# Performance work log

Measured on AMD Instinct MI355X. Metric: run time of the kernel, lower is better.

Reference implementation:

```python
import jax, jax.numpy as jnp
import numpy as np

HEAD_SIZE = 128
B, L = 4, 4096

def setup_inputs() -> dict:
    key = jax.random.key(0)
    k1, k2, k3 = jax.random.split(key, 3)
    return {
        "key": jax.random.normal(k1, (B, L, HEAD_SIZE), dtype=jnp.float32),
        "query": jax.random.normal(k2, (B, L, HEAD_SIZE), dtype=jnp.float32),
        "value": jax.random.normal(k3, (B, L, HEAD_SIZE), dtype=jnp.float32),
    }

def reference(key, query, value):
    # attention scores: [B, L, L]
    scale = 1.0 / jnp.sqrt(jnp.asarray(HEAD_SIZE, dtype=query.dtype))
    att = jnp.einsum("bqd,bkd->bqk", query, key) * scale
    # causal mask (tril): positions k > q get -inf
    causal = jnp.tril(jnp.ones((att.shape[1], att.shape[2]), dtype=bool))
    att = jnp.where(causal[None, :, :], att, jnp.array(-jnp.inf, dtype=att.dtype))
    logits = jax.nn.softmax(att, axis=-1)
    # dropout omitted (eval mode / deterministic reference)
    out = jnp.einsum("bqk,bkd->bqd", logits, value)
    return out
```

## Files before the change

### kernel.cpp

```cpp
#include <hip/hip_runtime.h>

#define BB 4
#define LL 4096
#define DD 128

typedef __attribute__((ext_vector_type(8))) short short8;
typedef __attribute__((ext_vector_type(4))) float f32x4;

typedef __attribute__((address_space(1))) const unsigned int gas_u32;
typedef __attribute__((address_space(3))) unsigned int las_u32;

__device__ __forceinline__ void gload_lds16(const void* g, void* l) {
  __builtin_amdgcn_global_load_lds((gas_u32*)g, (las_u32*)l, 16, 0, 0);
}

__device__ __forceinline__ unsigned short f2bf(float x) {
  union { float f; unsigned int u; } c; c.f = x;
  unsigned int r = (c.u + 0x7FFFu + ((c.u >> 16) & 1u)) >> 16;
  return (unsigned short)r;
}
__device__ __forceinline__ float bf2f(unsigned short h) {
  union { unsigned int u; float f; } c; c.u = (unsigned int)h << 16;
  return c.f;
}

__host__ __device__ __forceinline__ int slotBase(int p) {
  int g2 = (p - 4) >> 2, w2 = (p - 4) & 3;
  return 2 * g2 * g2 + 6 * g2 + w2 * (g2 + 2);
}

__global__ __launch_bounds__(256) void prep(const float* __restrict__ K,
                                            const float* __restrict__ V,
                                            unsigned short* __restrict__ Kb,
                                            unsigned short* __restrict__ Vt) {
  __shared__ unsigned short tile[64 * 130];
  int b  = blockIdx.x >> 6;
  int kt = (blockIdx.x & 63) << 6;
  int t = threadIdx.x;
  {
    int key = t >> 2, part = t & 3;
    const float* src = K + ((size_t)b * LL + kt + key) * DD + part * 32;
    unsigned short* dst = Kb + ((size_t)b * LL + kt + key) * DD + part * 32;
#pragma unroll
    for (int j = 0; j < 4; ++j) {
      float4 x = *(const float4*)(src + j * 8);
      float4 y = *(const float4*)(src + j * 8 + 4);
      union { unsigned short h[8]; uint4 v; } o;
      o.h[0] = f2bf(x.x); o.h[1] = f2bf(x.y); o.h[2] = f2bf(x.z); o.h[3] = f2bf(x.w);
      o.h[4] = f2bf(y.x); o.h[5] = f2bf(y.y); o.h[6] = f2bf(y.z); o.h[7] = f2bf(y.w);
      *(uint4*)(dst + j * 8) = o.v;
    }
  }
  int keyi = t >> 5, dim = (t & 31) * 4;
#pragma unroll
  for (int j = 0; j < 8; ++j) {
    int key = keyi + j * 8;
    float4 x = *(const float4*)(V + ((size_t)b * LL + kt + key) * DD + dim);
    uint2 pk;
    pk.x = f2bf(x.x) | ((unsigned int)f2bf(x.y) << 16);
    pk.y = f2bf(x.z) | ((unsigned int)f2bf(x.w) << 16);
    *(uint2*)(tile + key * 130 + dim) = pk;
  }
  __syncthreads();
  int kg = (t & 7) * 8, d0 = t >> 3;
#pragma unroll
  for (int j = 0; j < 4; ++j) {
    int d = d0 + j * 32;
    union { unsigned short h[8]; uint4 v; } o;
#pragma unroll
    for (int i = 0; i < 8; ++i) o.h[i] = tile[(kg + i) * 130 + d];
    *(uint4*)(Vt + ((size_t)b * DD + d) * LL + kt + kg) = o.v;
  }
}

__global__ __launch_bounds__(256, 3) void attn_fwd(const float* __restrict__ Q,
                                                   const unsigned short* __restrict__ Kb,
                                                   const unsigned short* __restrict__ Vt,
                                                   float* __restrict__ Out,
                                                   unsigned short* __restrict__ partO,
                                                   float* __restrict__ stats,
                                                   int split) {
  __shared__ unsigned short Ks[64 * 128];
  __shared__ unsigned short Vs[128 * 64];
  __shared__ unsigned short Ps[4][32 * 72];

  int tid = threadIdx.x;
  int wave = tid >> 6;
  int lane = tid & 63;
  int l = lane & 15, gq = lane >> 4;
  int lx = l & 7;

  int rem = (int)blockIdx.x, p = 31, nch;
  while (true) {
    nch = split ? ((2 * p + 2 + 7) >> 3) : 1;
    int n = 4 * nch;
    if (rem < n) break;
    rem -= n; --p;
  }
  int b = rem / nch, c = rem % nch;
  int T = 2 * p + 2;
  int nIters = split ? min(8, T - c * 8) : T;
  int ktBase = c << 9;
  int q0w = (p << 7) + wave * 32;
  int wkend = q0w + 31;
  int slot = (split && nch > 1) ? (b * 140 + slotBase(p) + c) : 0;

  const float SC = 0.08838834764831845f * 1.4426950408889634f;
  short8 qf[2][4];
#pragma unroll
  for (int mt = 0; mt < 2; ++mt) {
    const float* qp = Q + ((size_t)b * LL + q0w + mt * 16 + l) * DD + gq * 8;
#pragma unroll
    for (int cc = 0; cc < 4; ++cc) {
      float4 x = *(const float4*)(qp + cc * 32);
      float4 y = *(const float4*)(qp + cc * 32 + 4);
      short8 f;
      f[0] = (short)f2bf(x.x * SC); f[1] = (short)f2bf(x.y * SC);
      f[2] = (short)f2bf(x.z * SC); f[3] = (short)f2bf(x.w * SC);
      f[4] = (short)f2bf(y.x * SC); f[5] = (short)f2bf(y.y * SC);
      f[6] = (short)f2bf(y.z * SC); f[7] = (short)f2bf(y.w * SC);
      qf[mt][cc] = f;
    }
  }

  f32x4 acc[2][8];
#pragma unroll
  for (int mt = 0; mt < 2; ++mt)
#pragma unroll
    for (int i = 0; i < 8; ++i) acc[mt][i] = (f32x4){0.f, 0.f, 0.f, 0.f};
  f32x4 den[2];
  den[0] = (f32x4){0.f, 0.f, 0.f, 0.f};
  den[1] = (f32x4){0.f, 0.f, 0.f, 0.f};

  short8 ones;
#pragma unroll
  for (int j = 0; j < 8; ++j) ones[j] = (short)0x3F80;

  unsigned short* Pw = Ps[wave];
  const unsigned short* kgbase = Kb + (size_t)b * LL * DD;
  const unsigned short* vgbase = Vt + (size_t)b * DD * LL;

  for (int it = 0; it < nIters; ++it) {
    int kt = ktBase + it * 64;

    __syncthreads();
#pragma unroll
    for (int j = 0; j < 4; ++j) {
      int pk_ = j * 256 + tid;
      int krow = pk_ >> 4;
      int kcol = (pk_ & 15) ^ (krow & 7);
      gload_lds16(kgbase + (size_t)(kt + krow) * DD + kcol * 8, &Ks[pk_ * 8]);
      int vrow = pk_ >> 3;
      int vcol = (pk_ & 7) ^ (vrow & 7);
      gload_lds16(vgbase + (size_t)vrow * LL + kt + vcol * 8, &Vs[pk_ * 8]);
    }
    __syncthreads();

    if (kt > wkend) continue;

    bool diag = (kt + 63 > q0w);

#pragma unroll
    for (int nt = 0; nt < 4; ++nt) {
      const unsigned short* kp = Ks + (nt * 16 + l) * 128;
      f32x4 a0 = (f32x4){0.f, 0.f, 0.f, 0.f};
      f32x4 a1 = (f32x4){0.f, 0.f, 0.f, 0.f};
#pragma unroll
      for (int cc = 0; cc < 4; ++cc) {
        short8 kf = *(const short8*)(kp + (((gq + 4 * cc) ^ lx) << 3));
        a0 = __builtin_amdgcn_mfma_f32_16x16x32_bf16(qf[0][cc], kf, a0, 0, 0, 0);
        a1 = __builtin_amdgcn_mfma_f32_16x16x32_bf16(qf[1][cc], kf, a1, 0, 0, 0);
      }
      if (diag) {
        int key = kt + nt * 16 + l;
        int qr0 = q0w + gq * 4, qr1 = q0w + 16 + gq * 4;
#pragma unroll
        for (int r = 0; r < 4; ++r) {
          if (key > qr0 + r) a0[r] = -1e30f;
          if (key > qr1 + r) a1[r] = -1e30f;
        }
      }
#pragma unroll
      for (int r = 0; r < 4; ++r) {
        Pw[(gq * 4 + r) * 72 + nt * 16 + l] = f2bf(exp2f(a0[r]));
        Pw[(16 + gq * 4 + r) * 72 + nt * 16 + l] = f2bf(exp2f(a1[r]));
      }
    }

#pragma unroll
    for (int kc = 0; kc < 2; ++kc) {
      short8 pa0 = *(const short8*)(Pw + l * 72 + kc * 32 + gq * 8);
      short8 pa1 = *(const short8*)(Pw + (16 + l) * 72 + kc * 32 + gq * 8);
      den[0] = __builtin_amdgcn_mfma_f32_16x16x32_bf16(pa0, ones, den[0], 0, 0, 0);
      den[1] = __builtin_amdgcn_mfma_f32_16x16x32_bf16(pa1, ones, den[1], 0, 0, 0);
#pragma unroll
      for (int dt = 0; dt < 8; ++dt) {
        short8 vb = *(const short8*)(Vs + (dt * 16 + l) * 64 + (((kc * 4 + gq) ^ lx) << 3));
        acc[0][dt] = __builtin_amdgcn_mfma_f32_16x16x32_bf16(pa0, vb, acc[0][dt], 0, 0, 0);
        acc[1][dt] = __builtin_amdgcn_mfma_f32_16x16x32_bf16(pa1, vb, acc[1][dt], 0, 0, 0);
      }
    }
  }

  if (!split || nch == 1) {
    float* op = Out + ((size_t)b * LL + q0w) * DD;
#pragma unroll
    for (int mt = 0; mt < 2; ++mt) {
      float inv[4];
#pragma unroll
      for (int r = 0; r < 4; ++r) inv[r] = 1.0f / den[mt][r];
#pragma unroll
      for (int dt = 0; dt < 8; ++dt)
#pragma unroll
        for (int r = 0; r < 4; ++r)
          op[(size_t)(mt * 16 + gq * 4 + r) * DD + dt * 16 + l] = acc[mt][dt][r] * inv[r];
    }
  } else {
    unsigned short* pp = partO + (size_t)slot * 16384;
#pragma unroll
    for (int mt = 0; mt < 2; ++mt) {
      int rb = wave * 32 + mt * 16;
#pragma unroll
      for (int dt = 0; dt < 8; ++dt)
#pragma unroll
        for (int r = 0; r < 4; ++r)
          pp[(rb + gq * 4 + r) * 128 + dt * 16 + l] = f2bf(acc[mt][dt][r]);
      if (l == 0) {
#pragma unroll
        for (int r = 0; r < 4; ++r)
          stats[(size_t)slot * 128 + rb + gq * 4 + r] = den[mt][r];
      }
    }
  }
}

__global__ __launch_bounds__(256) void merge(const unsigned short* __restrict__ partO,
                                             const float* __restrict__ stats,
                                             float* __restrict__ Out) {
  int b = blockIdx.x / 112;
  int rest = blockIdx.x % 112;
  int p = 4 + rest / 4;
  int rg = rest % 4;
  int nch = (2 * p + 2 + 7) >> 3;
  int slot0 = b * 140 + slotBase(p);

  int tid = threadIdx.x;
  int row = rg * 32 + (tid >> 3);
  int dcol = (tid & 7) * 16;

  float lsum = 0.f;
  for (int cc = 0; cc < nch; ++cc)
    lsum += stats[(size_t)(slot0 + cc) * 128 + row];
  float inv = 1.0f / lsum;

  float o[16];
#pragma unroll
  for (int j = 0; j < 16; ++j) o[j] = 0.f;
  for (int cc = 0; cc < nch; ++cc) {
    const unsigned short* pp = partO + (size_t)(slot0 + cc) * 16384 + (size_t)row * 128 + dcol;
#pragma unroll
    for (int j = 0; j < 16; ++j) o[j] += bf2f(pp[j]);
  }
  float* op = Out + ((size_t)b * LL + (p << 7) + row) * DD + dcol;
#pragma unroll
  for (int j = 0; j < 4; ++j) {
    float4 v; v.x = o[j*4] * inv; v.y = o[j*4+1] * inv; v.z = o[j*4+2] * inv; v.w = o[j*4+3] * inv;
    *(float4*)(op + j * 4) = v;
  }
}

extern "C" void kernel_launch(void* const* d_in, const int* in_sizes, int n_in,
                              void* d_out, int out_size, void* d_ws, size_t ws_size,
                              hipStream_t stream) {
  const float* K = (const float*)d_in[0];
  const float* Q = (const float*)d_in[1];
  const float* V = (const float*)d_in[2];
  float* Out = (float*)d_out;

  const size_t convBytes = (size_t)2 * BB * LL * DD * 2;
  unsigned short* Kb = (unsigned short*)d_ws;
  unsigned short* Vt = Kb + (size_t)BB * LL * DD;

  size_t slots = (size_t)BB * 140;
  size_t need = convBytes + slots * 16384 * 2 + slots * 128 * 4;
  int split = (ws_size >= need) ? 1 : 0;

  unsigned short* partO = (unsigned short*)((char*)d_ws + convBytes);
  float* stats = (float*)((char*)d_ws + convBytes + slots * 16384 * 2);

  int nBlocks = 0;
  for (int p = 0; p < 32; ++p) nBlocks += 4 * (split ? ((2 * p + 2 + 7) >> 3) : 1);

  prep<<<dim3(BB * (LL / 64)), dim3(256), 0, stream>>>(K, V, Kb, Vt);
  attn_fwd<<<dim3(nBlocks), dim3(256), 0, stream>>>(Q, Kb, Vt, Out, partO, stats, split);
  if (split)
    merge<<<dim3(BB * 112), dim3(256), 0, stream>>>(partO, stats, Out);
}
```

Baseline: 121.8 us.

## Fuse split-K merge into attention kernel via last-block atomic counter

Removes the separate merge kernel launch. Each split chunk block atomically increments a per-(batch, query-tile) counter after writing its partial output and stats, and the last block to finish performs the reduction and normalization. Counters are zeroed in the prep kernel. The P-tile bf16 conversion now uses a packed two-float conversion intrinsic, and merge loads are vectorized. This saves a launch and the gap between kernels, at the cost of threadfence and atomic overhead and a serialized tail reduction in the last block.

```diff
diff --git a/kernel.cpp b/kernel.cpp
--- a/kernel.cpp
+++ b/kernel.cpp
@@ -1,4 +1,5 @@
 #include <hip/hip_runtime.h>
+#include <hip/hip_bf16.h>
 
 #define BB 4
 #define LL 4096
@@ -23,6 +24,12 @@
   union { unsigned int u; float f; } c; c.u = (unsigned int)h << 16;
   return c.f;
 }
+__device__ __forceinline__ unsigned int pk2bf(float a, float b) {
+  __hip_bfloat162 h = __float22bfloat162_rn(make_float2(a, b));
+  unsigned int u;
+  __builtin_memcpy(&u, &h, sizeof(u));
+  return u;
+}
 
 __host__ __device__ __forceinline__ int slotBase(int p) {
   int g2 = (p - 4) >> 2, w2 = (p - 4) & 3;
@@ -32,11 +39,13 @@
 __global__ __launch_bounds__(256) void prep(const float* __restrict__ K,
                                             const float* __restrict__ V,
                                             unsigned short* __restrict__ Kb,
-                                            unsigned short* __restrict__ Vt) {
+                                            unsigned short* __restrict__ Vt,
+                                            int* __restrict__ counters) {
   __shared__ unsigned short tile[64 * 130];
   int b  = blockIdx.x >> 6;
   int kt = (blockIdx.x & 63) << 6;
   int t = threadIdx.x;
+  if (blockIdx.x == 0 && t < BB * 32) counters[t] = 0;
   {
     int key = t >> 2, part = t & 3;
     const float* src = K + ((size_t)b * LL + kt + key) * DD + part * 32;
@@ -79,10 +88,12 @@
                                                    float* __restrict__ Out,
                                                    unsigned short* __restrict__ partO,
                                                    float* __restrict__ stats,
+                                                   int* __restrict__ counters,
                                                    int split) {
   __shared__ unsigned short Ks[64 * 128];
   __shared__ unsigned short Vs[128 * 64];
   __shared__ unsigned short Ps[4][32 * 72];
+  __shared__ int lastFlag;
 
   int tid = threadIdx.x;
   int wave = tid >> 6;
@@ -91,7 +102,7 @@
   int lx = l & 7;
 
   int rem = (int)blockIdx.x, p = 31, nch;
-  while (true) {
+  for (;;) {
     nch = split ? ((2 * p + 2 + 7) >> 3) : 1;
     int n = 4 * nch;
     if (rem < n) break;
@@ -103,7 +114,9 @@
   int ktBase = c << 9;
   int q0w = (p << 7) + wave * 32;
   int wkend = q0w + 31;
-  int slot = (split && nch > 1) ? (b * 140 + slotBase(p) + c) : 0;
+  int multi = (split && nch > 1);
+  int slot0 = multi ? (b * 140 + slotBase(p)) : 0;
+  int slot = slot0 + c;
 
   const float SC = 0.08838834764831845f * 1.4426950408889634f;
   short8 qf[2][4];
@@ -182,8 +195,9 @@
       }
 #pragma unroll
       for (int r = 0; r < 4; ++r) {
-        Pw[(gq * 4 + r) * 72 + nt * 16 + l] = f2bf(exp2f(a0[r]));
-        Pw[(16 + gq * 4 + r) * 72 + nt * 16 + l] = f2bf(exp2f(a1[r]));
+        unsigned int pk = pk2bf(exp2f(a0[r]), exp2f(a1[r]));
+        Pw[(gq * 4 + r) * 72 + nt * 16 + l] = (unsigned short)pk;
+        Pw[(16 + gq * 4 + r) * 72 + nt * 16 + l] = (unsigned short)(pk >> 16);
       }
     }
 
@@ -202,7 +216,7 @@
     }
   }
 
-  if (!split || nch == 1) {
+  if (!multi) {
     float* op = Out + ((size_t)b * LL + q0w) * DD;
 #pragma unroll
     for (int mt = 0; mt < 2; ++mt) {
@@ -215,57 +229,64 @@
         for (int r = 0; r < 4; ++r)
           op[(size_t)(mt * 16 + gq * 4 + r) * DD + dt * 16 + l] = acc[mt][dt][r] * inv[r];
     }
-  } else {
-    unsigned short* pp = partO + (size_t)slot * 16384;
-#pragma unroll
-    for (int mt = 0; mt < 2; ++mt) {
-      int rb = wave * 32 + mt * 16;
-#pragma unroll
-      for (int dt = 0; dt < 8; ++dt)
-#pragma unroll
-        for (int r = 0; r < 4; ++r)
-          pp[(rb + gq * 4 + r) * 128 + dt * 16 + l] = f2bf(acc[mt][dt][r]);
-      if (l == 0) {
-#pragma unroll
-        for (int r = 0; r < 4; ++r)
-          stats[(size_t)slot * 128 + rb + gq * 4 + r] = den[mt][r];
-      }
-    }
-  }
-}
-
-__global__ __launch_bounds__(256) void merge(const unsigned short* __restrict__ partO,
-                                             const float* __restrict__ stats,
-                                             float* __restrict__ Out) {
-  int b = blockIdx.x / 112;
-  int rest = blockIdx.x % 112;
-  int p = 4 + rest / 4;
-  int rg = rest % 4;
-  int nch = (2 * p + 2 + 7) >> 3;
-  int slot0 = b * 140 + slotBase(p);
-
-  int tid = threadIdx.x;
-  int row = rg * 32 + (tid >> 3);
-  int dcol = (tid & 7) * 16;
-
-  float lsum = 0.f;
-  for (int cc = 0; cc < nch; ++cc)
-    lsum += stats[(size_t)(slot0 + cc) * 128 + row];
-  float inv = 1.0f / lsum;
-
-  float o[16];
-#pragma unroll
-  for (int j = 0; j < 16; ++j) o[j] = 0.f;
-  for (int cc = 0; cc < nch; ++cc) {
-    const unsigned short* pp = partO + (size_t)(slot0 + cc) * 16384 + (size_t)row * 128 + dcol;
-#pragma unroll
-    for (int j = 0; j < 16; ++j) o[j] += bf2f(pp[j]);
-  }
-  float* op = Out + ((size_t)b * LL + (p << 7) + row) * DD + dcol;
-#pragma unroll
-  for (int j = 0; j < 4; ++j) {
-    float4 v; v.x = o[j*4] * inv; v.y = o[j*4+1] * inv; v.z = o[j*4+2] * inv; v.w = o[j*4+3] * inv;
-    *(float4*)(op + j * 4) = v;
+    return;
+  }
+
+  unsigned short* pp = partO + (size_t)slot * 16384;
+#pragma unroll
+  for (int mt = 0; mt < 2; ++mt) {
+    int rb = wave * 32 + mt * 16;
+#pragma unroll
+    for (int dt = 0; dt < 8; ++dt)
+#pragma unroll
+      for (int r = 0; r < 4; ++r)
+        pp[(rb + gq * 4 + r) * 128 + dt * 16 + l] = f2bf(acc[mt][dt][r]);
+    if (l == 0) {
+#pragma unroll
+      for (int r = 0; r < 4; ++r)
+        stats[(size_t)slot * 128 + rb + gq * 4 + r] = den[mt][r];
+    }
+  }
+
+  __threadfence();
+  __syncthreads();
+  if (tid == 0) {
+    int old = atomicAdd(&counters[b * 32 + p], 1);
+    lastFlag = (old == nch - 1);
+  }
+  __syncthreads();
+  if (!lastFlag) return;
+  __threadfence();
+
+#pragma unroll
+  for (int rg = 0; rg < 4; ++rg) {
+    int row = rg * 32 + (tid >> 3);
+    int dcol = (tid & 7) * 16;
+    float lsum = 0.f;
+    for (int cc = 0; cc < nch; ++cc)
+      lsum += stats[(size_t)(slot0 + cc) * 128 + row];
+    float inv = 1.0f / lsum;
+    float o[16];
+#pragma unroll
+    for (int j = 0; j < 16; ++j) o[j] = 0.f;
+    for (int cc = 0; cc < nch; ++cc) {
+      const unsigned short* q2 = partO + (size_t)(slot0 + cc) * 16384 + (size_t)row * 128 + dcol;
+      uint4 u0 = *(const uint4*)q2;
+      uint4 u1 = *(const uint4*)(q2 + 8);
+      const unsigned int uu[8] = {u0.x, u0.y, u0.z, u0.w, u1.x, u1.y, u1.z, u1.w};
+#pragma unroll
+      for (int j = 0; j < 8; ++j) {
+        o[j * 2]     += bf2f((unsigned short)uu[j]);
+        o[j * 2 + 1] += bf2f((unsigned short)(uu[j] >> 16));
+      }
+    }
+    float* op = Out + ((size_t)b * LL + (p << 7) + row) * DD + dcol;
+#pragma unroll
+    for (int j = 0; j < 4; ++j) {
+      float4 v4; v4.x = o[j*4] * inv; v4.y = o[j*4+1] * inv;
+      v4.z = o[j*4+2] * inv; v4.w = o[j*4+3] * inv;
+      *(float4*)(op + j * 4) = v4;
+    }
   }
 }
 
@@ -282,17 +303,16 @@
   unsigned short* Vt = Kb + (size_t)BB * LL * DD;
 
   size_t slots = (size_t)BB * 140;
-  size_t need = convBytes + slots * 16384 * 2 + slots * 128 * 4;
+  size_t need = convBytes + slots * 32768 + slots * 512 + 512;
   int split = (ws_size >= need) ? 1 : 0;
 
   unsigned short* partO = (unsigned short*)((char*)d_ws + convBytes);
-  float* stats = (float*)((char*)d_ws + convBytes + slots * 16384 * 2);
+  float* stats = (float*)((char*)d_ws + convBytes + slots * 32768);
+  int* counters = (int*)((char*)d_ws + convBytes + slots * 32768 + slots * 512);
 
   int nBlocks = 0;
   for (int p = 0; p < 32; ++p) nBlocks += 4 * (split ? ((2 * p + 2 + 7) >> 3) : 1);
 
-  prep<<<dim3(BB * (LL / 64)), dim3(256), 0, stream>>>(K, V, Kb, Vt);
-  attn_fwd<<<dim3(nBlocks), dim3(256), 0, stream>>>(Q, Kb, Vt, Out, partO, stats, split);
-  if (split)
-    merge<<<dim3(BB * 112), dim3(256), 0, stream>>>(partO, stats, Out);
-}
+  prep<<<dim3(BB * (LL / 64)), dim3(256), 0, stream>>>(K, V, Kb, Vt, counters);
+  attn_fwd<<<dim3(nBlocks), dim3(256), 0, stream>>>(Q, Kb, Vt, Out, partO, stats, counters, split);
+}
```

Result: slower. 223.7 us (+83.7%).
